# Performance work log

Measured on AMD Instinct MI355X. Metric: run time of the kernel, lower is better.

The kernel has to match this reference:

```python
import jax, jax.numpy as jnp
import numpy as np

B, C, T, H, W, E, K = 2, 256, 16, 32, 32, 4, 2


def setup_inputs() -> dict:
    key = jax.random.key(0)
    ks = jax.random.split(key, 5)
    x = jax.random.normal(ks[0], (B, C, T, H, W), dtype=jnp.float32)
    # gate: Conv3d(dim, E, 1) -> weight [E, C], bias [E]
    gate_w = jax.random.normal(ks[1], (E, C), dtype=jnp.float32) * 0.02
    gate_b = jnp.zeros((E,), dtype=jnp.float32)
    # experts_layer1: Conv3d(dim, dim*E, 1) -> weight [E*C, C], bias [E*C]
    w1 = jax.random.normal(ks[2], (E * C, C), dtype=jnp.float32) * 0.02
    b1 = jnp.zeros((E * C,), dtype=jnp.float32)
    # experts_layer2: Conv3d(dim*E, dim*E, 1, groups=E) -> per-expert [C, C]
    w2 = jax.random.normal(ks[3], (E, C, C), dtype=jnp.float32) * 0.02
    b2 = jnp.zeros((E, C), dtype=jnp.float32)
    return {"x": x, "gate_w": gate_w, "gate_b": gate_b,
            "w1": w1, "b1": b1, "w2": w2, "b2": b2}


def reference(x, gate_w, gate_b, w1, b1, w2, b2):
    # gating: 1x1x1 conv == channel contraction; logits [B,T,H,W,E]
    logits = jnp.einsum('bcthw,ec->bthwe', x, gate_w) + gate_b
    vals, idx = jax.lax.top_k(logits, K)              # [B,T,H,W,K]
    wk = jax.nn.softmax(vals, axis=-1).astype(x.dtype)
    # scatter top-k softmax weights back into E slots (zeros elsewhere)
    weights = jnp.sum(jax.nn.one_hot(idx, E, dtype=x.dtype) * wk[..., None],
                      axis=-2)                        # [B,T,H,W,E]
    # layer1 (dense 1x1x1 conv) + SiLU; output channels = E*C
    h = jax.nn.silu(jnp.einsum('bcthw,oc->bothw', x, w1)
                    + b1[None, :, None, None, None])
    h = h.reshape(B, E, C, T, H, W)
    # layer2: grouped 1x1x1 conv, one [C,C] matmul per expert
    expert_out = (jnp.einsum('becthw,eoc->beothw', h, w2)
                  + b2[None, :, :, None, None, None])  # [B,E,C,T,H,W]
    # weighted combine over experts + residual
    out = jnp.einsum('becthw,bthwe->bcthw', expert_out, weights)
    return out + x
```

## Files before the change

### kernel.cpp

```cpp
#include <hip/hip_runtime.h>
#include <hip/hip_bf16.h>


#define C_DIM 256
#define S_DIM 16384
#define E_DIM 4
#define MT 64
#define XST 264
#define OST 68
#define WFRAG_ELEMS 262144

typedef __attribute__((ext_vector_type(8))) short bf16x8;
typedef __attribute__((ext_vector_type(4))) float f32x4;

__device__ __forceinline__ short bfq(float f) {
  __hip_bfloat16 h = __float2bfloat16(f);
  return *(short*)&h;
}

__global__ __launch_bounds__(256) void prepack_kernel(
    const float* __restrict__ w1, const float* __restrict__ w2,
    __hip_bfloat16* __restrict__ dst)
{
  int o8 = blockIdx.x * 256 + threadIdx.x;
  int o  = o8 << 3;
  int half = o >> 18;
  int idx  = o & (WFRAG_ELEMS - 1);
  int lane = (idx >> 3) & 63;
  int kc   = (idx >> 9) & 7;
  int nt   = (idx >> 12) & 15;
  int e    = (idx >> 16) & 3;
  const float* src = half ? w2 : w1;
  const float* s = src + (e*256 + nt*16 + (lane & 15))*256 + kc*32 + (lane >> 4)*8;
  const float4 v0 = *(const float4*)s;
  const float4 v1 = *(const float4*)(s + 4);
  bf16x8 outv = {bfq(v0.x), bfq(v0.y), bfq(v0.z), bfq(v0.w),
                 bfq(v1.x), bfq(v1.y), bfq(v1.z), bfq(v1.w)};
  *(bf16x8*)((short*)dst + o) = outv;
}

template<int MTC>
__device__ __forceinline__ void gemm1_sparse(
    const short* XsS, short* HsS, const short* w1e, const float* b1e,
    const unsigned char* plist_e, const float* wgtg_e,
    int wv, int r, int q, bool dosync)
{
  f32x4 hacc[MTC][2];
#pragma unroll
  for (int i = 0; i < MTC; ++i)
#pragma unroll
    for (int j = 0; j < 2; ++j) hacc[i][j] = (f32x4){0.f, 0.f, 0.f, 0.f};

  int aoff[MTC];
#pragma unroll
  for (int Mt = 0; Mt < MTC; ++Mt)
    aoff[Mt] = (int)plist_e[Mt*16 + r] * XST;

  bf16x8 bw[2][2];
#pragma unroll
  for (int t = 0; t < 2; ++t) bw[0][t] = *(const bf16x8*)(w1e + (t*8 + 0)*512);
#pragma unroll
  for (int kc = 0; kc < 8; ++kc) {
    if (kc < 7) {
#pragma unroll
      for (int t = 0; t < 2; ++t)
        bw[(kc+1)&1][t] = *(const bf16x8*)(w1e + (t*8 + kc + 1)*512);
    }
    bf16x8 a[MTC];
#pragma unroll
    for (int Mt = 0; Mt < MTC; ++Mt)
      a[Mt] = *(const bf16x8*)(XsS + aoff[Mt] + kc*32 + q*8);
#pragma unroll
    for (int Mt = 0; Mt < MTC; ++Mt)
#pragma unroll
      for (int t = 0; t < 2; ++t)
        hacc[Mt][t] = __builtin_amdgcn_mfma_f32_16x16x32_bf16(a[Mt], bw[kc&1][t], hacc[Mt][t], 0, 0, 0);
  }

  if (dosync) __syncthreads();

#pragma unroll
  for (int Mt = 0; Mt < MTC; ++Mt) {
    const int g0 = Mt*16 + q*4;
    const unsigned pw = *(const unsigned*)(plist_e + g0);
    const f32x4 wg = *(const f32x4*)(wgtg_e + g0);
#pragma unroll
    for (int t = 0; t < 2; ++t) {
      const int n = wv*32 + t*16 + r;
      const float bias = b1e[n];
#pragma unroll
      for (int reg = 0; reg < 4; ++reg) {
        const int p = (pw >> (8*reg)) & 255;
        const float z = hacc[Mt][t][reg] + bias;
        const float s = __builtin_amdgcn_rcpf(1.0f + __expf(-z));
        HsS[p*XST + n] = bfq(z * s * wg[reg]);
      }
    }
  }
}

__global__ __launch_bounds__(512, 4) void moe_fused_kernel(
    const float* __restrict__ x,
    const float* __restrict__ gate_w,
    const float* __restrict__ gate_b,
    const float* __restrict__ b1,
    const float* __restrict__ b2,
    const __hip_bfloat16* __restrict__ wp,
    float* __restrict__ out)
{
  __shared__ __align__(16) char pool[256 * OST * 4];
  __shared__ __align__(16) float Wgt[MT * 4];
  __shared__ __align__(16) unsigned char plist[4][64];
  __shared__ __align__(16) float WgtG[4][64];
  __shared__ __align__(4)  unsigned char zlist[4][64];
  __shared__ int mcnt[4];

  short* XsS = (short*)pool;
  short* HsS = (short*)(pool + MT * XST * 2);
  float* Os  = (float*)pool;

  const int tid  = threadIdx.x;
  const int lane = tid & 63;
  const int wv   = tid >> 6;
  const int r    = lane & 15;
  const int q    = lane >> 4;

  const int g  = blockIdx.x;
  const int b  = g >> 8;
  const int s0 = (g & 255) * MT;
  const float* xb = x + (size_t)b * C_DIM * S_DIM + s0;

  {
    const int p  = lane;
    const int c0 = wv * 32;
    float xv[32];
#pragma unroll
    for (int j = 0; j < 32; ++j)
      xv[j] = xb[(size_t)(c0 + j) * S_DIM + p];

    double acc[4] = {0.0, 0.0, 0.0, 0.0};
#pragma unroll
    for (int j = 0; j < 32; ++j) {
      const double xd = (double)xv[j];
      acc[0] += xd * (double)gate_w[0*256 + c0 + j];
      acc[1] += xd * (double)gate_w[1*256 + c0 + j];
      acc[2] += xd * (double)gate_w[2*256 + c0 + j];
      acc[3] += xd * (double)gate_w[3*256 + c0 + j];
    }

#pragma unroll
    for (int k = 0; k < 4; ++k) {
      bf16x8 blk = {bfq(xv[k*8+0]), bfq(xv[k*8+1]), bfq(xv[k*8+2]), bfq(xv[k*8+3]),
                    bfq(xv[k*8+4]), bfq(xv[k*8+5]), bfq(xv[k*8+6]), bfq(xv[k*8+7])};
      *(bf16x8*)(XsS + p*XST + c0 + k*8) = blk;
    }

    double* GateD = (double*)HsS;
#pragma unroll
    for (int e = 0; e < 4; ++e)
      GateD[(e*8 + wv)*64 + p] = acc[e];
  }
  __syncthreads();

  if (tid < 256) {
    const int p = tid >> 2;
    const int e = tid & 3;
    const double* GateD = (const double*)HsS;
    double s = (double)gate_b[e];
#pragma unroll
    for (int g2 = 0; g2 < 8; ++g2) s += GateD[(e*8 + g2)*64 + p];
    const float la = (float)s;
    const float lb = __shfl_xor(la, 1, 64);
    const float lc = __shfl_xor(la, 2, 64);
    const float ld = __shfl_xor(lb, 2, 64);
    if (e == 0) {
      const float l0 = la, l1 = lb, l2 = lc, l3 = ld;
      int i1 = 0; float v1 = l0;
      if (l1 > v1) { v1 = l1; i1 = 1; }
      if (l2 > v1) { v1 = l2; i1 = 2; }
      if (l3 > v1) { v1 = l3; i1 = 3; }
      float v2 = -3.0e38f; int i2 = 0;
      if (i1 != 0 && l0 > v2) { v2 = l0; i2 = 0; }
      if (i1 != 1 && l1 > v2) { v2 = l1; i2 = 1; }
      if (i1 != 2 && l2 > v2) { v2 = l2; i2 = 2; }
      if (i1 != 3 && l3 > v2) { v2 = l3; i2 = 3; }
      const float wA = 1.0f / (1.0f + __expf(v2 - v1));
      const float wB = 1.0f - wA;
      f32x4 w;
      w[0] = (i1 == 0) ? wA : ((i2 == 0) ? wB : 0.0f);
      w[1] = (i1 == 1) ? wA : ((i2 == 1) ? wB : 0.0f);
      w[2] = (i1 == 2) ? wA : ((i2 == 2) ? wB : 0.0f);
      w[3] = (i1 == 3) ? wA : ((i2 == 3) ? wB : 0.0f);
      *(f32x4*)(&Wgt[p*4]) = w;
    }
  }
  __syncthreads();

  if (wv < 4) {
    const int e = wv;
    const int p = lane;
    const float w = Wgt[p*4 + e];
    const bool sel = (w != 0.0f);
    const unsigned long long mask = __ballot(sel);
    const int below = __popcll(mask & ((1ull << p) - 1ull));
    const int m = __popcll(mask);
    const int pad = (((m + 15) >> 4) << 4) - m;
    if (sel) {
      plist[e][below] = (unsigned char)p;
      WgtG[e][below]  = w;
    } else {
      const int zidx = p - below;
      zlist[e][zidx] = (unsigned char)p;
      if (zidx < pad) {
        plist[e][m + zidx] = (unsigned char)p;
        WgtG[e][m + zidx]  = 0.0f;
      }
    }
    if (p == 0) mcnt[e] = m;
  }
  __syncthreads();

  const short* W1P = (const short*)wp;
  const short* W2P = (const short*)wp + WFRAG_ELEMS;

  f32x4 oacc[4][2];
#pragma unroll
  for (int i = 0; i < 4; ++i)
#pragma unroll
    for (int j = 0; j < 2; ++j) oacc[i][j] = (f32x4){0.f, 0.f, 0.f, 0.f};

  for (int e = 0; e < E_DIM; ++e) {
    const int me = mcnt[e];
    const int mt = __builtin_amdgcn_readfirstlane((me + 15) >> 4);
    const short* w1e = W1P + ((e*16 + wv*2)*8)*512 + lane*8;
    const float* b1e = b1 + e*256;
    const bool dosync = (e > 0);

    if      (mt == 2) gemm1_sparse<2>(XsS, HsS, w1e, b1e, plist[e], WgtG[e], wv, r, q, dosync);
    else if (mt == 3) gemm1_sparse<3>(XsS, HsS, w1e, b1e, plist[e], WgtG[e], wv, r, q, dosync);
    else if (mt == 4) gemm1_sparse<4>(XsS, HsS, w1e, b1e, plist[e], WgtG[e], wv, r, q, dosync);
    else if (mt == 1) gemm1_sparse<1>(XsS, HsS, w1e, b1e, plist[e], WgtG[e], wv, r, q, dosync);
    else { if (dosync) __syncthreads(); }

    const short* w2e = W2P + ((e*16 + wv*2)*8)*512 + lane*8;
    bf16x8 cw[2][2];
#pragma unroll
    for (int t = 0; t < 2; ++t) cw[0][t] = *(const bf16x8*)(w2e + (t*8 + 0)*512);

    {
      const int zm = 64 - me;
      const bf16x8 zz = {0,0,0,0,0,0,0,0};
      for (int i = tid; i < zm*32; i += 512) {
        const int row = zlist[e][i >> 5];
        *(bf16x8*)(HsS + row*XST + (i & 31)*8) = zz;
      }
    }
    __syncthreads();

    {
#pragma unroll
      for (int kc = 0; kc < 8; ++kc) {
        if (kc < 7) {
#pragma unroll
          for (int t = 0; t < 2; ++t)
            cw[(kc+1)&1][t] = *(const bf16x8*)(w2e + (t*8 + kc + 1)*512);
        }
        bf16x8 a[4];
#pragma unroll
        for (int Mt = 0; Mt < 4; ++Mt)
          a[Mt] = *(const bf16x8*)(HsS + (Mt*16 + r)*XST + kc*32 + q*8);
#pragma unroll
        for (int Mt = 0; Mt < 4; ++Mt)
#pragma unroll
          for (int t = 0; t < 2; ++t)
            oacc[Mt][t] = __builtin_amdgcn_mfma_f32_16x16x32_bf16(a[Mt], cw[kc&1][t], oacc[Mt][t], 0, 0, 0);
      }
    }
  }
  __syncthreads();

  {
    float b2v[2][4];
#pragma unroll
    for (int t = 0; t < 2; ++t) {
      const int c = wv*32 + t*16 + r;
#pragma unroll
      for (int e = 0; e < 4; ++e) b2v[t][e] = b2[e*256 + c];
    }
#pragma unroll
    for (int Mt = 0; Mt < 4; ++Mt) {
      f32x4 wv4[4];
#pragma unroll
      for (int reg = 0; reg < 4; ++reg)
        wv4[reg] = *(const f32x4*)(&Wgt[(Mt*16 + q*4 + reg)*4]);
#pragma unroll
      for (int t = 0; t < 2; ++t) {
        f32x4 v = oacc[Mt][t];
#pragma unroll
        for (int reg = 0; reg < 4; ++reg)
          v[reg] += wv4[reg][0]*b2v[t][0] + wv4[reg][1]*b2v[t][1]
                  + wv4[reg][2]*b2v[t][2] + wv4[reg][3]*b2v[t][3];
        *(f32x4*)(Os + (size_t)(wv*32 + t*16 + r)*OST + Mt*16 + q*4) = v;
      }
    }
  }
  __syncthreads();

  {
    const int p4 = (tid & 15) * 4;
    const int cg = tid >> 4;
    float* ob = out + (size_t)b * C_DIM * S_DIM + s0;
#pragma unroll
    for (int cc = 0; cc < 8; ++cc) {
      const int c = cc*32 + cg;
      const f32x4  o  = *(const f32x4*)(Os + (size_t)c*OST + p4);
      const float4 xr = *(const float4*)(xb + (size_t)c*S_DIM + p4);
      float4 res;
      res.x = o[0] + xr.x; res.y = o[1] + xr.y;
      res.z = o[2] + xr.z; res.w = o[3] + xr.w;
      *(float4*)(ob + (size_t)c*S_DIM + p4) = res;
    }
  }
}

extern "C" void kernel_launch(void* const* d_in, const int* in_sizes, int n_in,
                              void* d_out, int out_size, void* d_ws, size_t ws_size,
                              hipStream_t stream)
{
  (void)in_sizes; (void)n_in; (void)out_size; (void)ws_size;
  const float* x      = (const float*)d_in[0];
  const float* gate_w = (const float*)d_in[1];
  const float* gate_b = (const float*)d_in[2];
  const float* w1     = (const float*)d_in[3];
  const float* b1     = (const float*)d_in[4];
  const float* w2     = (const float*)d_in[5];
  const float* b2     = (const float*)d_in[6];
  float* out = (float*)d_out;
  __hip_bfloat16* wpack = (__hip_bfloat16*)d_ws;

  prepack_kernel<<<256, 256, 0, stream>>>(w1, w2, wpack);
  moe_fused_kernel<<<512, 512, 0, stream>>>(x, gate_w, gate_b, b1, b2, wpack, out);
}
```

Baseline: 126.4 us.

## Halve spatial tile to 32 positions, double grid, coalesce weight prepack reads

Reduces the per-block spatial tile from 64 to 32 positions, doubling the grid to 1024 blocks and raising the launch-bounds occupancy hint to 8 blocks per CU. The aim is more parallelism and smaller shared memory and register use per block, which should improve latency hiding on the many CUs. The prepack kernel is also reindexed so each thread reads contiguous source rows and scatters into the fragment layout, giving coalesced global reads. In exchange, each block reloads the full expert weights for half as many positions, doubling weight traffic per output, and each wave does less MFMA work per weight fragment.

```diff
diff --git a/kernel.cpp b/kernel.cpp
--- a/kernel.cpp
+++ b/kernel.cpp
@@ -5,9 +5,9 @@
 #define C_DIM 256
 #define S_DIM 16384
 #define E_DIM 4
-#define MT 64
+#define MT 32
 #define XST 264
-#define OST 68
+#define OST 36
 #define WFRAG_ELEMS 262144
 
 typedef __attribute__((ext_vector_type(8))) short bf16x8;
@@ -22,21 +22,25 @@
     const float* __restrict__ w1, const float* __restrict__ w2,
     __hip_bfloat16* __restrict__ dst)
 {
-  int o8 = blockIdx.x * 256 + threadIdx.x;
-  int o  = o8 << 3;
-  int half = o >> 18;
-  int idx  = o & (WFRAG_ELEMS - 1);
-  int lane = (idx >> 3) & 63;
-  int kc   = (idx >> 9) & 7;
-  int nt   = (idx >> 12) & 15;
-  int e    = (idx >> 16) & 3;
+  int o8   = blockIdx.x * 256 + threadIdx.x;
+  int half = o8 >> 15;
+  int idx  = o8 & 32767;
+  int j    = idx & 31;
+  int rowid= idx >> 5;
+  int e    = rowid >> 8;
+  int nt   = (rowid >> 4) & 15;
+  int row  = rowid & 15;
+  int kc   = j >> 2;
+  int col8 = j & 3;
+  int lane = (col8 << 4) | row;
   const float* src = half ? w2 : w1;
-  const float* s = src + (e*256 + nt*16 + (lane & 15))*256 + kc*32 + (lane >> 4)*8;
+  const float* s = src + rowid * 256 + j * 8;
   const float4 v0 = *(const float4*)s;
   const float4 v1 = *(const float4*)(s + 4);
   bf16x8 outv = {bfq(v0.x), bfq(v0.y), bfq(v0.z), bfq(v0.w),
                  bfq(v1.x), bfq(v1.y), bfq(v1.z), bfq(v1.w)};
-  *(bf16x8*)((short*)dst + o) = outv;
+  int chunk = ((e*16 + nt)*8 + kc)*64 + lane;
+  *(bf16x8*)((short*)dst + half*WFRAG_ELEMS + chunk*8) = outv;
 }
 
 template<int MTC>
@@ -99,7 +103,7 @@
   }
 }
 
-__global__ __launch_bounds__(512, 4) void moe_fused_kernel(
+__global__ __launch_bounds__(512, 8) void moe_fused_kernel(
     const float* __restrict__ x,
     const float* __restrict__ gate_w,
     const float* __restrict__ gate_b,
@@ -110,9 +114,9 @@
 {
   __shared__ __align__(16) char pool[256 * OST * 4];
   __shared__ __align__(16) float Wgt[MT * 4];
-  __shared__ __align__(16) unsigned char plist[4][64];
-  __shared__ __align__(16) float WgtG[4][64];
-  __shared__ __align__(4)  unsigned char zlist[4][64];
+  __shared__ __align__(16) unsigned char plist[4][32];
+  __shared__ __align__(16) float WgtG[4][32];
+  __shared__ __align__(4)  unsigned char zlist[4][32];
   __shared__ int mcnt[4];
 
   short* XsS = (short*)pool;
@@ -126,21 +130,22 @@
   const int q    = lane >> 4;
 
   const int g  = blockIdx.x;
-  const int b  = g >> 8;
-  const int s0 = (g & 255) * MT;
+  const int b  = g >> 9;
+  const int s0 = (g & 511) * MT;
   const float* xb = x + (size_t)b * C_DIM * S_DIM + s0;
 
   {
-    const int p  = lane;
-    const int c0 = wv * 32;
-    float xv[32];
-#pragma unroll
-    for (int j = 0; j < 32; ++j)
+    const int p  = lane & 31;
+    const int h  = lane >> 5;
+    const int c0 = wv * 32 + h * 16;
+    float xv[16];
+#pragma unroll
+    for (int j = 0; j < 16; ++j)
       xv[j] = xb[(size_t)(c0 + j) * S_DIM + p];
 
     double acc[4] = {0.0, 0.0, 0.0, 0.0};
 #pragma unroll
-    for (int j = 0; j < 32; ++j) {
+    for (int j = 0; j < 16; ++j) {
       const double xd = (double)xv[j];
       acc[0] += xd * (double)gate_w[0*256 + c0 + j];
       acc[1] += xd * (double)gate_w[1*256 + c0 + j];
@@ -149,7 +154,7 @@
     }
 
 #pragma unroll
-    for (int k = 0; k < 4; ++k) {
+    for (int k = 0; k < 2; ++k) {
       bf16x8 blk = {bfq(xv[k*8+0]), bfq(xv[k*8+1]), bfq(xv[k*8+2]), bfq(xv[k*8+3]),
                     bfq(xv[k*8+4]), bfq(xv[k*8+5]), bfq(xv[k*8+6]), bfq(xv[k*8+7])};
       *(bf16x8*)(XsS + p*XST + c0 + k*8) = blk;
@@ -158,17 +163,17 @@
     double* GateD = (double*)HsS;
 #pragma unroll
     for (int e = 0; e < 4; ++e)
-      GateD[(e*8 + wv)*64 + p] = acc[e];
-  }
-  __syncthreads();
-
-  if (tid < 256) {
+      GateD[(e*16 + wv*2 + h)*32 + p] = acc[e];
+  }
+  __syncthreads();
+
+  if (tid < 128) {
     const int p = tid >> 2;
     const int e = tid & 3;
     const double* GateD = (const double*)HsS;
     double s = (double)gate_b[e];
 #pragma unroll
-    for (int g2 = 0; g2 < 8; ++g2) s += GateD[(e*8 + g2)*64 + p];
+    for (int g2 = 0; g2 < 16; ++g2) s += GateD[(e*16 + g2)*32 + p];
     const float la = (float)s;
     const float lb = __shfl_xor(la, 1, 64);
     const float lc = __shfl_xor(la, 2, 64);
@@ -199,21 +204,23 @@
   if (wv < 4) {
     const int e = wv;
     const int p = lane;
-    const float w = Wgt[p*4 + e];
+    const float w = (p < MT) ? Wgt[p*4 + e] : 0.0f;
     const bool sel = (w != 0.0f);
     const unsigned long long mask = __ballot(sel);
     const int below = __popcll(mask & ((1ull << p) - 1ull));
     const int m = __popcll(mask);
     const int pad = (((m + 15) >> 4) << 4) - m;
-    if (sel) {
-      plist[e][below] = (unsigned char)p;
-      WgtG[e][below]  = w;
-    } else {
-      const int zidx = p - below;
-      zlist[e][zidx] = (unsigned char)p;
-      if (zidx < pad) {
-        plist[e][m + zidx] = (unsigned char)p;
-        WgtG[e][m + zidx]  = 0.0f;
+    if (p < MT) {
+      if (sel) {
+        plist[e][below] = (unsigned char)p;
+        WgtG[e][below]  = w;
+      } else {
+        const int zidx = p - below;
+        zlist[e][zidx] = (unsigned char)p;
+        if (zidx < pad) {
+          plist[e][m + zidx] = (unsigned char)p;
+          WgtG[e][m + zidx]  = 0.0f;
+        }
       }
     }
     if (p == 0) mcnt[e] = m;
@@ -223,9 +230,9 @@
   const short* W1P = (const short*)wp;
   const short* W2P = (const short*)wp + WFRAG_ELEMS;
 
-  f32x4 oacc[4][2];
-#pragma unroll
-  for (int i = 0; i < 4; ++i)
+  f32x4 oacc[2][2];
+#pragma unroll
+  for (int i = 0; i < 2; ++i)
 #pragma unroll
     for (int j = 0; j < 2; ++j) oacc[i][j] = (f32x4){0.f, 0.f, 0.f, 0.f};
 
@@ -236,10 +243,8 @@
     const float* b1e = b1 + e*256;
     const bool dosync = (e > 0);
 
-    if      (mt == 2) gemm1_sparse<2>(XsS, HsS, w1e, b1e, plist[e], WgtG[e], wv, r, q, dosync);
-    else if (mt == 3) gemm1_sparse<3>(XsS, HsS, w1e, b1e, plist[e], WgtG[e], wv, r, q, dosync);
-    else if (mt == 4) gemm1_sparse<4>(XsS, HsS, w1e, b1e, plist[e], WgtG[e], wv, r, q, dosync);
-    else if (mt == 1) gemm1_sparse<1>(XsS, HsS, w1e, b1e, plist[e], WgtG[e], wv, r, q, dosync);
+    if      (mt == 1) gemm1_sparse<1>(XsS, HsS, w1e, b1e, plist[e], WgtG[e], wv, r, q, dosync);
+    else if (mt == 2) gemm1_sparse<2>(XsS, HsS, w1e, b1e, plist[e], WgtG[e], wv, r, q, dosync);
     else { if (dosync) __syncthreads(); }
 
     const short* w2e = W2P + ((e*16 + wv*2)*8)*512 + lane*8;
@@ -248,7 +253,7 @@
     for (int t = 0; t < 2; ++t) cw[0][t] = *(const bf16x8*)(w2e + (t*8 + 0)*512);
 
     {
-      const int zm = 64 - me;
+      const int zm = MT - me;
       const bf16x8 zz = {0,0,0,0,0,0,0,0};
       for (int i = tid; i < zm*32; i += 512) {
         const int row = zlist[e][i >> 5];
@@ -265,12 +270,12 @@
           for (int t = 0; t < 2; ++t)
             cw[(kc+1)&1][t] = *(const bf16x8*)(w2e + (t*8 + kc + 1)*512);
         }
-        bf16x8 a[4];
-#pragma unroll
-        for (int Mt = 0; Mt < 4; ++Mt)
+        bf16x8 a[2];
+#pragma unroll
+        for (int Mt = 0; Mt < 2; ++Mt)
           a[Mt] = *(const bf16x8*)(HsS + (Mt*16 + r)*XST + kc*32 + q*8);
 #pragma unroll
-        for (int Mt = 0; Mt < 4; ++Mt)
+        for (int Mt = 0; Mt < 2; ++Mt)
 #pragma unroll
           for (int t = 0; t < 2; ++t)
             oacc[Mt][t] = __builtin_amdgcn_mfma_f32_16x16x32_bf16(a[Mt], cw[kc&1][t], oacc[Mt][t], 0, 0, 0);
@@ -288,7 +293,7 @@
       for (int e = 0; e < 4; ++e) b2v[t][e] = b2[e*256 + c];
     }
 #pragma unroll
-    for (int Mt = 0; Mt < 4; ++Mt) {
+    for (int Mt = 0; Mt < 2; ++Mt) {
       f32x4 wv4[4];
 #pragma unroll
       for (int reg = 0; reg < 4; ++reg)
@@ -307,12 +312,12 @@
   __syncthreads();
 
   {
-    const int p4 = (tid & 15) * 4;
-    const int cg = tid >> 4;
+    const int p4 = (tid & 7) * 4;
+    const int cg = tid >> 3;
     float* ob = out + (size_t)b * C_DIM * S_DIM + s0;
 #pragma unroll
-    for (int cc = 0; cc < 8; ++cc) {
-      const int c = cc*32 + cg;
+    for (int cc = 0; cc < 4; ++cc) {
+      const int c = cc*64 + cg;
       const f32x4  o  = *(const f32x4*)(Os + (size_t)c*OST + p4);
       const float4 xr = *(const float4*)(xb + (size_t)c*S_DIM + p4);
       float4 res;
@@ -339,5 +344,5 @@
   __hip_bfloat16* wpack = (__hip_bfloat16*)d_ws;
 
   prepack_kernel<<<256, 256, 0, stream>>>(w1, w2, wpack);
-  moe_fused_kernel<<<512, 512, 0, stream>>>(x, gate_w, gate_b, b1, b2, wpack, out);
-}
+  moe_fused_kernel<<<1024, 512, 0, stream>>>(x, gate_w, gate_b, b1, b2, wpack, out);
+}
```

After: 180.8 us. +43.1%, slower.
